# Kernel tuning notes

Measured on AMD Instinct MI355X. Metric: run time of the kernel, lower is better.

Reference implementation:

```python
import jax, jax.numpy as jnp
import numpy as np

H = 1024          # hidden_size
E = 2 * H         # expansion e
S_DIM = 128       # shared q/k dim s
B, S = 4, 2048


def setup_inputs() -> dict:
    key = jax.random.key(0)
    ks = jax.random.split(key, 6)
    inputs = jax.random.normal(ks[0], (B, S, H), dtype=jnp.float32)
    W_uv = jax.random.normal(ks[1], (H, 2 * E + S_DIM), dtype=jnp.float32) * (1.0 / np.sqrt(H))
    b_uv = jnp.zeros((2 * E + S_DIM,), dtype=jnp.float32)
    gamma = jax.random.normal(ks[2], (2, S_DIM), dtype=jnp.float32) * 0.02
    beta = jnp.zeros((2, S_DIM), dtype=jnp.float32)
    W_out = jax.random.normal(ks[3], (E, H), dtype=jnp.float32) * (1.0 / np.sqrt(E))
    b_out = jnp.zeros((H,), dtype=jnp.float32)
    return {"inputs": inputs, "W_uv": W_uv, "b_uv": b_uv,
            "gamma": gamma, "beta": beta, "W_out": W_out, "b_out": b_out}


def reference(inputs, W_uv, b_uv, gamma, beta, W_out, b_out):
    seq_len = inputs.shape[1]
    # uv projection + SiLU
    uvb = jax.nn.silu(jnp.einsum('bsh,hf->bsf', inputs, W_uv) + b_uv)
    u = uvb[..., :E]                       # [B,S,E]
    v = uvb[..., E:2 * E]                  # [B,S,E]
    base = uvb[..., 2 * E:]                # [B,S,s]
    # per-head affine: [B,S,1,s]*[2,s] + [2,s] -> [B,S,2,s]
    qk = base[..., None, :] * gamma + beta
    q, k = qk[..., 0, :], qk[..., 1, :]    # [B,S,s] each
    scores = jnp.einsum('bns,bms->bnm', q, k) / seq_len   # [B,S,S]
    sq = jnp.square(jax.nn.relu(scores))
    attn_v = jnp.einsum('bnm,bme->bne', sq, v)            # [B,S,E]
    return jnp.einsum('bne,eh->bnh', u * attn_v, W_out) + b_out
```

## Files before the change

kernel.cpp:

```cpp
#include <hip/hip_runtime.h>
#include <stdint.h>


#define H_DIM  1024
#define E_DIM  2048
#define SD     128
#define B_SZ   4
#define S_LEN  2048
#define M_TOT  (B_SZ * S_LEN)
#define F_DIM  (2 * E_DIM + SD)

typedef _Float16 f16;
typedef __attribute__((ext_vector_type(4))) _Float16 f16x4;
typedef __attribute__((ext_vector_type(8))) _Float16 f16x8;
typedef __attribute__((ext_vector_type(16))) float f32x16;

__device__ __forceinline__ float silu_f(float x) { return x / (1.f + __expf(-x)); }

__device__ __forceinline__ void gload16(const void* g, void* l) {
  __builtin_amdgcn_global_load_lds(
      (const __attribute__((address_space(1))) void*)(uintptr_t)g,
      (__attribute__((address_space(3))) void*)(uint32_t)(uintptr_t)l,
      16, 0, 0);
}

__global__ __launch_bounds__(256) void cast_f16_k(const float* __restrict__ src,
                                                  f16* __restrict__ dst, long n) {
  long i = ((long)blockIdx.x * 256 + threadIdx.x) * 4;
  if (i < n) {
    float4 v = *(const float4*)(src + i);
    f16x4 h; h[0] = (f16)v.x; h[1] = (f16)v.y; h[2] = (f16)v.z; h[3] = (f16)v.w;
    *(f16x4*)(dst + i) = h;
  }
}

__global__ __launch_bounds__(256) void transpose_cast_k(const float* __restrict__ src,
                                                        f16* __restrict__ dst, int R, int C) {
  __shared__ float tile[32][33];
  int c0 = blockIdx.x * 32, r0 = blockIdx.y * 32;
  int tx = threadIdx.x & 31, ty = threadIdx.x >> 5;
  for (int i = ty; i < 32; i += 8) tile[i][tx] = src[(long)(r0 + i) * C + c0 + tx];
  __syncthreads();
  for (int i = ty; i < 32; i += 8) dst[(long)(c0 + i) * R + r0 + tx] = (f16)tile[tx][i];
}

template <int MODE>
__global__ __launch_bounds__(256) void mfma_gemm(
    const f16* __restrict__ Ag, const f16* __restrict__ Bg,
    float* __restrict__ F0, f16* __restrict__ H0, const f16* __restrict__ H1,
    f16* __restrict__ H2, f16* __restrict__ H3,
    const float* __restrict__ C0, const float* __restrict__ C1,
    const float* __restrict__ C2)
{
  constexpr int K   = (MODE == 1) ? SD : (MODE == 0 || MODE == 4) ? H_DIM : 2048;
  constexpr int LDA = K, LDB = K;

  __shared__ f16 As[2][128][32];
  __shared__ f16 Bs[2][128][32];

  const int t    = threadIdx.x;
  const int w    = t >> 6;
  const int lane = t & 63;
  const int lo5  = lane & 31;
  const int hi   = lane >> 5;
  const int wy   = w >> 1, wx = w & 1;
  const int m0   = blockIdx.y * 128;
  const int n0   = blockIdx.x * 128;
  const long z   = blockIdx.z;

  const f16* A = Ag + (MODE == 1 ? z * (long)S_LEN * SD
                     : MODE == 2 ? z * (long)S_LEN * S_LEN : 0);
  const f16* B = Bg + (MODE == 1 ? z * (long)S_LEN * SD
                     : MODE == 2 ? z * (long)E_DIM * S_LEN : 0);

  const int srow = lane >> 2;
  const int scol = (((lane & 3) ^ ((srow >> 1) & 3))) * 8;
  const int rsw  = (lo5 >> 1) & 3;

  f32x16 acc[2][2] = {};

  for (int k0 = 0; k0 < K; k0 += 64) {
#pragma unroll
    for (int h = 0; h < 2; h++)
#pragma unroll
      for (int g16 = 0; g16 < 2; g16++) {
        const int r = (w << 5) + (g16 << 4);
        gload16(A + (long)(m0 + r + srow) * LDA + k0 + (h << 5) + scol, &As[h][r][0]);
        gload16(B + (long)(n0 + r + srow) * LDB + k0 + (h << 5) + scol, &Bs[h][r][0]);
      }
    __syncthreads();

#pragma unroll
    for (int ks = 0; ks < 4; ks++) {
      const int h  = ks >> 1;
      const int cl = ((ks & 1) << 1) + hi;
      const int kc = (cl ^ rsw) << 3;
      f16x8 av[2], bv[2];
#pragma unroll
      for (int i = 0; i < 2; i++)
        av[i] = *(const f16x8*)&As[h][(wy << 6) + (i << 5) + lo5][kc];
#pragma unroll
      for (int j = 0; j < 2; j++)
        bv[j] = *(const f16x8*)&Bs[h][(wx << 6) + (j << 5) + lo5][kc];
#pragma unroll
      for (int i = 0; i < 2; i++)
#pragma unroll
        for (int j = 0; j < 2; j++)
          acc[i][j] = __builtin_amdgcn_mfma_f32_32x32x16_f16(av[i], bv[j], acc[i][j], 0, 0, 0);
    }
    __syncthreads();
  }

  const int rb0 = m0 + (wy << 6) + (hi << 2);
  const int cb0 = n0 + (wx << 6) + lo5;

  if (MODE == 0) {
    if (n0 < E_DIM) {
#pragma unroll
      for (int i = 0; i < 2; i++)
#pragma unroll
        for (int j = 0; j < 2; j++) {
          int gc = cb0 + (j << 5);
          float bias = C0[gc];
#pragma unroll
          for (int g = 0; g < 4; g++)
#pragma unroll
            for (int rr = 0; rr < 4; rr++) {
              int gr = rb0 + (i << 5) + (g << 3) + rr;
              H0[(long)gr * E_DIM + gc] = (f16)silu_f(acc[i][j][g * 4 + rr] + bias);
            }
        }
    } else {
#pragma unroll
      for (int i = 0; i < 2; i++) {
#pragma unroll
        for (int j = 0; j < 2; j++) {
          int gc = cb0 + (j << 5);
          float bias = C0[gc];
#pragma unroll
          for (int g = 0; g < 4; g++) {
            int gr0 = rb0 + (i << 5) + (g << 3);
            int b   = gr0 >> 11;
            int s0  = gr0 & (S_LEN - 1);
            f16x4 pk;
#pragma unroll
            for (int rr = 0; rr < 4; rr++) pk[rr] = (f16)silu_f(acc[i][j][g * 4 + rr] + bias);
            *(f16x4*)&H1[((long)b * E_DIM + (gc - E_DIM)) * S_LEN + s0] = pk;
          }
        }
      }
    }
  } else if (MODE == 4) {
#pragma unroll
    for (int i = 0; i < 2; i++)
#pragma unroll
      for (int j = 0; j < 2; j++) {
        int jj = cb0 + (j << 5);
        float bias = C0[jj];
        float g0 = C1[jj], g1 = C1[SD + jj];
        float be0 = C2[jj], be1 = C2[SD + jj];
#pragma unroll
        for (int g = 0; g < 4; g++)
#pragma unroll
          for (int rr = 0; rr < 4; rr++) {
            int gr = rb0 + (i << 5) + (g << 3) + rr;
            float s = silu_f(acc[i][j][g * 4 + rr] + bias);
            H2[(long)gr * SD + jj] = (f16)(s * g0 + be0);
            H3[(long)gr * SD + jj] = (f16)(s * g1 + be1);
          }
      }
  } else if (MODE == 1) {
#pragma unroll
    for (int i = 0; i < 2; i++)
#pragma unroll
      for (int j = 0; j < 2; j++) {
        int gc = cb0 + (j << 5);
#pragma unroll
        for (int g = 0; g < 4; g++)
#pragma unroll
          for (int rr = 0; rr < 4; rr++) {
            int gr = rb0 + (i << 5) + (g << 3) + rr;
            float tv = fmaxf(acc[i][j][g * 4 + rr], 0.f) * 64.f;
            H0[z * (long)S_LEN * S_LEN + (long)gr * S_LEN + gc] = (f16)(tv * tv);
          }
      }
  } else if (MODE == 2) {
    const long rowoff = z * S_LEN;
#pragma unroll
    for (int i = 0; i < 2; i++)
#pragma unroll
      for (int j = 0; j < 2; j++) {
        int gc = cb0 + (j << 5);
#pragma unroll
        for (int g = 0; g < 4; g++)
#pragma unroll
          for (int rr = 0; rr < 4; rr++) {
            int gr = rb0 + (i << 5) + (g << 3) + rr;
            long idx = (rowoff + gr) * (long)E_DIM + gc;
            H0[idx] = (f16)((float)H1[idx] * acc[i][j][g * 4 + rr]);
          }
      }
  } else {
#pragma unroll
    for (int i = 0; i < 2; i++)
#pragma unroll
      for (int j = 0; j < 2; j++) {
        int gc = cb0 + (j << 5);
        float bias = C0[gc];
#pragma unroll
        for (int g = 0; g < 4; g++)
#pragma unroll
          for (int rr = 0; rr < 4; rr++) {
            int gr = rb0 + (i << 5) + (g << 3) + rr;
            F0[(long)gr * H_DIM + gc] = acc[i][j][g * 4 + rr] * (1.0f / 17179869184.0f) + bias;
          }
      }
  }
}

extern "C" void kernel_launch(void* const* d_in, const int* in_sizes, int n_in,
                              void* d_out, int out_size, void* d_ws, size_t ws_size,
                              hipStream_t stream) {
  const float* X     = (const float*)d_in[0];
  const float* W_uv  = (const float*)d_in[1];
  const float* b_uv  = (const float*)d_in[2];
  const float* gamma = (const float*)d_in[3];
  const float* beta  = (const float*)d_in[4];
  const float* W_out = (const float*)d_in[5];
  const float* b_out = (const float*)d_in[6];
  float* out = (float*)d_out;

  char* wp = (char*)d_ws;
  f16* Xh   = (f16*)wp; wp += (long)M_TOT * H_DIM * 2;
  f16* Wuvt = (f16*)wp; wp += (long)F_DIM * H_DIM * 2;
  f16* Wt   = (f16*)wp; wp += (long)H_DIM * E_DIM * 2;
  f16* u    = (f16*)wp; wp += (long)M_TOT * E_DIM * 2;
  f16* vt   = (f16*)wp; wp += (long)M_TOT * E_DIM * 2;
  f16* qh   = (f16*)wp; wp += (long)M_TOT * SD * 2;
  f16* kh   = (f16*)wp; wp += (long)M_TOT * SD * 2;
  f16* sq   = (f16*)wp; wp += (long)B_SZ * S_LEN * S_LEN * 2;
  f16* p    = (f16*)wp; wp += (long)M_TOT * E_DIM * 2;

  cast_f16_k<<<(M_TOT * H_DIM) / (256 * 4), 256, 0, stream>>>(X, Xh, (long)M_TOT * H_DIM);
  transpose_cast_k<<<dim3(F_DIM / 32, H_DIM / 32), 256, 0, stream>>>(W_uv, Wuvt, H_DIM, F_DIM);
  transpose_cast_k<<<dim3(H_DIM / 32, E_DIM / 32), 256, 0, stream>>>(W_out, Wt, E_DIM, H_DIM);

  mfma_gemm<0><<<dim3(2 * E_DIM / 128, M_TOT / 128, 1), 256, 0, stream>>>(
      Xh, Wuvt, nullptr, u, vt, nullptr, nullptr, b_uv, nullptr, nullptr);

  mfma_gemm<4><<<dim3(1, M_TOT / 128, 1), 256, 0, stream>>>(
      Xh, Wuvt + (long)2 * E_DIM * H_DIM, nullptr, nullptr, nullptr, qh, kh,
      b_uv + 2 * E_DIM, gamma, beta);

  mfma_gemm<1><<<dim3(S_LEN / 128, S_LEN / 128, B_SZ), 256, 0, stream>>>(
      qh, kh, nullptr, sq, nullptr, nullptr, nullptr, nullptr, nullptr, nullptr);

  mfma_gemm<2><<<dim3(E_DIM / 128, S_LEN / 128, B_SZ), 256, 0, stream>>>(
      sq, vt, nullptr, p, u, nullptr, nullptr, nullptr, nullptr, nullptr);

  mfma_gemm<3><<<dim3(H_DIM / 128, M_TOT / 128, 1), 256, 0, stream>>>(
      p, Wt, out, nullptr, nullptr, nullptr, nullptr, b_out, nullptr, nullptr);
}
```

Measured before the change: 398.0 us.

## Add 256x256-tile pipelined GEMM kernel for the three large matmuls

Adds a new gemm256 kernel using 512 threads, 256x256 output tiles, and 64-wide K slices, with double-buffered LDS staged through global_load_lds. It overlaps loads and MFMA across four sub-phases using explicit vmcnt waits, barriers and setprio, and remaps workgroups with an XCD-aware swizzle. The uv projection, attention-times-v, and output projection GEMMs switch to this kernel, and the old mfma_gemm drops those modes. Larger tiles raise data reuse and cut global traffic, at the cost of more LDS (128KB per block) and more registers, which may limit occupancy.

```diff
diff --git a/kernel.cpp b/kernel.cpp
--- a/kernel.cpp
+++ b/kernel.cpp
@@ -45,6 +45,159 @@
 }
 
 template <int MODE>
+__global__ __launch_bounds__(512, 2) void gemm256(
+    const f16* __restrict__ Ag, const f16* __restrict__ Bg,
+    float* __restrict__ F0, f16* __restrict__ O0, f16* __restrict__ O1,
+    const f16* __restrict__ I0, const float* __restrict__ C0)
+{
+  constexpr int K  = (MODE == 0) ? H_DIM : 2048;
+  constexpr int NT = K / 64;
+
+  __shared__ f16 As[2][256][64];
+  __shared__ f16 Bs[2][256][64];
+
+  const int t    = threadIdx.x;
+  const int w    = t >> 6;
+  const int lane = t & 63;
+  const int lo5  = lane & 31;
+  const int hi   = lane >> 5;
+  const int wm   = w >> 2;
+  const int wn   = w & 3;
+
+  const int gx  = gridDim.x;
+  const int nwg = gx * gridDim.y;
+  const int lin = blockIdx.y * gx + blockIdx.x;
+  const int cpx = nwg >> 3;
+  const int wg  = (lin & 7) * cpx + (lin >> 3);
+  const int n0  = (wg % gx) * 256;
+  const int m0  = (wg / gx) * 256;
+  const long z  = blockIdx.z;
+
+  const f16* A = Ag + (MODE == 2 ? z * (long)S_LEN * S_LEN : 0);
+  const f16* B = Bg + (MODE == 2 ? z * (long)E_DIM * S_LEN : 0);
+
+  auto stageA = [&](int bb, int half, int kt2) {
+    const f16* g0 = A + (long)(m0 + half * 128) * K + kt2 * 64;
+    f16* lb = &As[bb][half * 128][0];
+#pragma unroll
+    for (int j = 0; j < 2; j++) {
+      int grp = (j << 3) + w;
+      int rl  = (grp << 3) + (lane >> 3);
+      gload16(g0 + (long)rl * K + (((lane & 7) ^ (lane >> 3)) << 3), lb + (grp << 9));
+    }
+  };
+  auto stageB = [&](int bb, int half, int kt2) {
+    const f16* g0 = B + (long)(n0 + half * 128) * K + kt2 * 64;
+    f16* lb = &Bs[bb][half * 128][0];
+#pragma unroll
+    for (int j = 0; j < 2; j++) {
+      int grp = (j << 3) + w;
+      int rl  = (grp << 3) + (lane >> 3);
+      gload16(g0 + (long)rl * K + (((lane & 7) ^ (lane >> 3)) << 3), lb + (grp << 9));
+    }
+  };
+
+  f32x16 acc[4][2] = {};
+
+  stageA(0, 0, 0); stageA(0, 1, 0); stageB(0, 0, 0); stageB(0, 1, 0);
+  stageB(1, 0, 1); stageA(1, 1, 1);
+  asm volatile("s_waitcnt vmcnt(4)" ::: "memory");
+  __builtin_amdgcn_s_barrier();
+
+#define PHASE(Q, MS, NS, STAGE_STMT, TAIL_STMT) do {                            \
+    f16x8 av0_[4], av1_[4], bv_[4];                                             \
+    const int ar_ = (MS) * 128 + wm * 64 + lo5;                                 \
+    const int br_ = (NS) * 128 + wn * 32 + lo5;                                 \
+    _Pragma("unroll")                                                           \
+    for (int ksl = 0; ksl < 4; ksl++) {                                         \
+      const int pc_ = (((ksl << 1) + hi) ^ (lo5 & 7)) << 3;                     \
+      av0_[ksl] = *(const f16x8*)&As[bf][ar_][pc_];                             \
+      av1_[ksl] = *(const f16x8*)&As[bf][ar_ + 32][pc_];                        \
+      bv_[ksl]  = *(const f16x8*)&Bs[bf][br_][pc_];                             \
+    }                                                                           \
+    STAGE_STMT;                                                                 \
+    __builtin_amdgcn_s_barrier();                                               \
+    __builtin_amdgcn_s_setprio(1);                                              \
+    _Pragma("unroll")                                                           \
+    for (int ksl = 0; ksl < 4; ksl++) {                                         \
+      acc[Q][0] = __builtin_amdgcn_mfma_f32_32x32x16_f16(av0_[ksl], bv_[ksl],   \
+                                                         acc[Q][0], 0, 0, 0);   \
+      acc[Q][1] = __builtin_amdgcn_mfma_f32_32x32x16_f16(av1_[ksl], bv_[ksl],   \
+                                                         acc[Q][1], 0, 0, 0);   \
+    }                                                                           \
+    __builtin_amdgcn_s_setprio(0);                                              \
+    TAIL_STMT;                                                                  \
+    __builtin_amdgcn_s_barrier();                                               \
+  } while (0)
+
+  for (int kt = 0; kt < NT; ++kt) {
+    const int bf = kt & 1;
+    const bool s1 = (kt + 1 < NT);
+    const bool s2 = (kt + 2 < NT);
+    PHASE(0, 0, 0, if (s1) { stageA(bf ^ 1, 0, kt + 1); stageB(bf ^ 1, 1, kt + 1); }, );
+    PHASE(1, 1, 0, , );
+    PHASE(2, 1, 1, if (s2) { stageB(bf, 0, kt + 2); }, );
+    PHASE(3, 0, 1, if (s2) { stageA(bf, 1, kt + 2); },
+          if (s2) { asm volatile("s_waitcnt vmcnt(4)" ::: "memory"); }
+          else    { asm volatile("s_waitcnt vmcnt(0)" ::: "memory"); });
+  }
+#undef PHASE
+
+#pragma unroll
+  for (int q = 0; q < 4; q++) {
+    const int ms = (q == 1 || q == 2) ? 1 : 0;
+    const int ns = q >> 1;
+#pragma unroll
+    for (int im = 0; im < 2; im++) {
+      const int gc    = n0 + ns * 128 + wn * 32 + lo5;
+      const int rbase = m0 + ms * 128 + wm * 64 + im * 32 + (hi << 2);
+      if (MODE == 0) {
+        const float bias = C0[gc];
+        if (n0 < E_DIM) {
+#pragma unroll
+          for (int g = 0; g < 4; g++)
+#pragma unroll
+            for (int rr = 0; rr < 4; rr++) {
+              int gr = rbase + (g << 3) + rr;
+              O0[(long)gr * E_DIM + gc] = (f16)silu_f(acc[q][im][g * 4 + rr] + bias);
+            }
+        } else {
+#pragma unroll
+          for (int g = 0; g < 4; g++) {
+            int gr0 = rbase + (g << 3);
+            int b   = gr0 >> 11;
+            int s0  = gr0 & (S_LEN - 1);
+            f16x4 pk;
+#pragma unroll
+            for (int rr = 0; rr < 4; rr++) pk[rr] = (f16)silu_f(acc[q][im][g * 4 + rr] + bias);
+            *(f16x4*)&O1[((long)b * E_DIM + (gc - E_DIM)) * S_LEN + s0] = pk;
+          }
+        }
+      } else if (MODE == 2) {
+        const long rowoff = z * S_LEN;
+#pragma unroll
+        for (int g = 0; g < 4; g++)
+#pragma unroll
+          for (int rr = 0; rr < 4; rr++) {
+            int gr = rbase + (g << 3) + rr;
+            long idx = (rowoff + gr) * (long)E_DIM + gc;
+            O0[idx] = (f16)((float)I0[idx] * acc[q][im][g * 4 + rr]);
+          }
+      } else {
+        const float bias = C0[gc];
+#pragma unroll
+        for (int g = 0; g < 4; g++)
+#pragma unroll
+          for (int rr = 0; rr < 4; rr++) {
+            int gr = rbase + (g << 3) + rr;
+            F0[(long)gr * H_DIM + gc] = acc[q][im][g * 4 + rr] * (1.0f / 17179869184.0f) + bias;
+          }
+      }
+    }
+  }
+}
+
+template <int MODE>
 __global__ __launch_bounds__(256) void mfma_gemm(
     const f16* __restrict__ Ag, const f16* __restrict__ Bg,
     float* __restrict__ F0, f16* __restrict__ H0, const f16* __restrict__ H1,
@@ -52,7 +205,7 @@
     const float* __restrict__ C0, const float* __restrict__ C1,
     const float* __restrict__ C2)
 {
-  constexpr int K   = (MODE == 1) ? SD : (MODE == 0 || MODE == 4) ? H_DIM : 2048;
+  constexpr int K   = (MODE == 1) ? SD : H_DIM;
   constexpr int LDA = K, LDB = K;
 
   __shared__ f16 As[2][128][32];
@@ -68,10 +221,8 @@
   const int n0   = blockIdx.x * 128;
   const long z   = blockIdx.z;
 
-  const f16* A = Ag + (MODE == 1 ? z * (long)S_LEN * SD
-                     : MODE == 2 ? z * (long)S_LEN * S_LEN : 0);
-  const f16* B = Bg + (MODE == 1 ? z * (long)S_LEN * SD
-                     : MODE == 2 ? z * (long)E_DIM * S_LEN : 0);
+  const f16* A = Ag + (MODE == 1 ? z * (long)S_LEN * SD : 0);
+  const f16* B = Bg + (MODE == 1 ? z * (long)S_LEN * SD : 0);
 
   const int srow = lane >> 2;
   const int scol = (((lane & 3) ^ ((srow >> 1) & 3))) * 8;
@@ -114,43 +265,7 @@
   const int rb0 = m0 + (wy << 6) + (hi << 2);
   const int cb0 = n0 + (wx << 6) + lo5;
 
-  if (MODE == 0) {
-    if (n0 < E_DIM) {
-#pragma unroll
-      for (int i = 0; i < 2; i++)
-#pragma unroll
-        for (int j = 0; j < 2; j++) {
-          int gc = cb0 + (j << 5);
-          float bias = C0[gc];
-#pragma unroll
-          for (int g = 0; g < 4; g++)
-#pragma unroll
-            for (int rr = 0; rr < 4; rr++) {
-              int gr = rb0 + (i << 5) + (g << 3) + rr;
-              H0[(long)gr * E_DIM + gc] = (f16)silu_f(acc[i][j][g * 4 + rr] + bias);
-            }
-        }
-    } else {
-#pragma unroll
-      for (int i = 0; i < 2; i++) {
-#pragma unroll
-        for (int j = 0; j < 2; j++) {
-          int gc = cb0 + (j << 5);
-          float bias = C0[gc];
-#pragma unroll
-          for (int g = 0; g < 4; g++) {
-            int gr0 = rb0 + (i << 5) + (g << 3);
-            int b   = gr0 >> 11;
-            int s0  = gr0 & (S_LEN - 1);
-            f16x4 pk;
-#pragma unroll
-            for (int rr = 0; rr < 4; rr++) pk[rr] = (f16)silu_f(acc[i][j][g * 4 + rr] + bias);
-            *(f16x4*)&H1[((long)b * E_DIM + (gc - E_DIM)) * S_LEN + s0] = pk;
-          }
-        }
-      }
-    }
-  } else if (MODE == 4) {
+  if (MODE == 4) {
 #pragma unroll
     for (int i = 0; i < 2; i++)
 #pragma unroll
@@ -169,7 +284,7 @@
             H3[(long)gr * SD + jj] = (f16)(s * g1 + be1);
           }
       }
-  } else if (MODE == 1) {
+  } else {
 #pragma unroll
     for (int i = 0; i < 2; i++)
 #pragma unroll
@@ -182,37 +297,6 @@
             int gr = rb0 + (i << 5) + (g << 3) + rr;
             float tv = fmaxf(acc[i][j][g * 4 + rr], 0.f) * 64.f;
             H0[z * (long)S_LEN * S_LEN + (long)gr * S_LEN + gc] = (f16)(tv * tv);
-          }
-      }
-  } else if (MODE == 2) {
-    const long rowoff = z * S_LEN;
-#pragma unroll
-    for (int i = 0; i < 2; i++)
-#pragma unroll
-      for (int j = 0; j < 2; j++) {
-        int gc = cb0 + (j << 5);
-#pragma unroll
-        for (int g = 0; g < 4; g++)
-#pragma unroll
-          for (int rr = 0; rr < 4; rr++) {
-            int gr = rb0 + (i << 5) + (g << 3) + rr;
-            long idx = (rowoff + gr) * (long)E_DIM + gc;
-            H0[idx] = (f16)((float)H1[idx] * acc[i][j][g * 4 + rr]);
-          }
-      }
-  } else {
-#pragma unroll
-    for (int i = 0; i < 2; i++)
-#pragma unroll
-      for (int j = 0; j < 2; j++) {
-        int gc = cb0 + (j << 5);
-        float bias = C0[gc];
-#pragma unroll
-        for (int g = 0; g < 4; g++)
-#pragma unroll
-          for (int rr = 0; rr < 4; rr++) {
-            int gr = rb0 + (i << 5) + (g << 3) + rr;
-            F0[(long)gr * H_DIM + gc] = acc[i][j][g * 4 + rr] * (1.0f / 17179869184.0f) + bias;
           }
       }
   }
@@ -245,8 +329,8 @@
   transpose_cast_k<<<dim3(F_DIM / 32, H_DIM / 32), 256, 0, stream>>>(W_uv, Wuvt, H_DIM, F_DIM);
   transpose_cast_k<<<dim3(H_DIM / 32, E_DIM / 32), 256, 0, stream>>>(W_out, Wt, E_DIM, H_DIM);
 
-  mfma_gemm<0><<<dim3(2 * E_DIM / 128, M_TOT / 128, 1), 256, 0, stream>>>(
-      Xh, Wuvt, nullptr, u, vt, nullptr, nullptr, b_uv, nullptr, nullptr);
+  gemm256<0><<<dim3(2 * E_DIM / 256, M_TOT / 256, 1), 512, 0, stream>>>(
+      Xh, Wuvt, nullptr, u, vt, nullptr, b_uv);
 
   mfma_gemm<4><<<dim3(1, M_TOT / 128, 1), 256, 0, stream>>>(
       Xh, Wuvt + (long)2 * E_DIM * H_DIM, nullptr, nullptr, nullptr, qh, kh,
@@ -255,9 +339,9 @@
   mfma_gemm<1><<<dim3(S_LEN / 128, S_LEN / 128, B_SZ), 256, 0, stream>>>(
       qh, kh, nullptr, sq, nullptr, nullptr, nullptr, nullptr, nullptr, nullptr);
 
-  mfma_gemm<2><<<dim3(E_DIM / 128, S_LEN / 128, B_SZ), 256, 0, stream>>>(
-      sq, vt, nullptr, p, u, nullptr, nullptr, nullptr, nullptr, nullptr);
-
-  mfma_gemm<3><<<dim3(H_DIM / 128, M_TOT / 128, 1), 256, 0, stream>>>(
-      p, Wt, out, nullptr, nullptr, nullptr, nullptr, b_out, nullptr, nullptr);
-}
+  gemm256<2><<<dim3(E_DIM / 256, S_LEN / 256, B_SZ), 512, 0, stream>>>(
+      sq, vt, nullptr, p, nullptr, u, nullptr);
+
+  gemm256<3><<<dim3(H_DIM / 256, M_TOT / 256, 1), 512, 0, stream>>>(
+      p, Wt, out, nullptr, nullptr, nullptr, b_out);
+}
```

Result: slower. 435.2 us (+9.3%).
